# Optimization experiments

Measured on AMD Instinct MI355X. Metric: run time of the kernel, lower is better.

Reference implementation:

```python
import jax, jax.numpy as jnp
import numpy as np
import math

B, T = 16, 512
P = 256          # num_memory_positions
E = 128          # embedding_dim
NB = 4           # num_beings
K = 4            # attention_radius
TEMP = 8.0       # attention_temperature
PHI = 1.618033988749895


def setup_inputs() -> dict:
    key = jax.random.key(0)
    ks = jax.random.split(key, 8)
    x = jax.random.normal(ks[0], (B, T, 8), jnp.float32)
    W_in = jax.random.normal(ks[1], (8, E), jnp.float32) * 0.1
    b_in = jnp.zeros((E,), jnp.float32)
    W_out = jax.random.normal(ks[2], (E, 8), jnp.float32) * 0.1
    b_out = jnp.zeros((8,), jnp.float32)
    W_p = jax.random.normal(ks[3], (E, E), jnp.float32) * (1.0 / np.sqrt(E))
    b_p = jnp.zeros((E,), jnp.float32)
    ptr_dest = jax.random.uniform(ks[4], (NB, P), jnp.float32) * P
    jump_W = jax.random.normal(ks[5], (NB, E), jnp.float32) * 0.1
    jump_b = jnp.zeros((NB,), jnp.float32)
    ctx_strength = jnp.full((NB,), 0.2, jnp.float32)
    pe = np.zeros((NB, E), np.float32)
    for i in range(NB):
        ph = i * PHI
        v = []
        for h in range(1, 9):
            v += [math.sin(h * ph), math.cos(h * ph)]
        pe[i, :16] = v  # phase_embedding padded with zeros to E (E >= 16)
    phase_bias = jnp.asarray(pe)
    seg = P / NB
    pointer_init = jax.random.uniform(ks[6], (NB, B), jnp.float32) * seg + jnp.arange(NB, dtype=jnp.float32)[:, None] * seg
    return dict(x=x, W_in=W_in, b_in=b_in, W_out=W_out, b_out=b_out,
                W_p=W_p, b_p=b_p, ptr_dest=ptr_dest, jump_W=jump_W,
                jump_b=jump_b, ctx_strength=ctx_strength,
                phase_bias=phase_bias, pointer_init=pointer_init)


def _forward(x, W_in, b_in, W_out, b_out, W_p, b_p, ptr_dest, jump_W,
             jump_b, ctx_strength, phase_bias, pointer_init):
    offsets = jnp.arange(-K, K + 1)          # [W]
    b_ix = jnp.arange(B)                     # [B]
    half = P / 2.0
    ring0 = jnp.zeros((B, P, E), x.dtype)
    hid0 = jnp.zeros((NB, B, E), x.dtype)

    def step(carry, x_t):
        ring, ptrs, hids = carry
        inp = x_t @ W_in + b_in              # [B,E]
        outs, new_ptrs, new_hids = [], [], []
        for i in range(NB):                  # beings sequential (share ring)
            ptr, hid = ptrs[i], hids[i]
            base = jnp.clip(jnp.floor(ptr).astype(jnp.int32), 0, P - 1)
            idx = (base[:, None] + offsets[None, :]) % P            # [B,W]
            delta = jnp.mod(idx.astype(x_t.dtype) - ptr[:, None] + half, P) - half
            w = jax.nn.softmax(-(delta ** 2) / TEMP, axis=1)         # [B,W]
            nbhd = ring[b_ix[:, None], idx]                          # [B,W,E]
            ctx = jnp.sum(w[..., None] * nbhd, axis=1)               # [B,E]
            comb = inp + jax.nn.sigmoid(ctx_strength[i]) * ctx + 0.1 * phase_bias[i]
            s = jnp.tanh(comb + hid)
            s = jnp.tanh(s @ W_p + b_p)      # depth-1 = 1 processing layer
            ring = ring.at[b_ix[:, None], idx].add(w[..., None] * s[:, None, :])
            cur = jnp.clip(ptr.astype(jnp.int32), 0, P - 1)
            jump_target = ptr_dest[i][cur]                           # [B]
            probs = jax.nn.sigmoid(s @ jump_W[i] + jump_b[i])        # [B]
            hard = (probs > 0.5).astype(s.dtype)
            should_jump = hard - jax.lax.stop_gradient(probs) + probs
            walk = (ptr + 1.0) % P
            new_ptrs.append(jnp.where(should_jump > 0.5, jump_target, walk))
            new_hids.append(s)
            outs.append(s @ W_out + b_out)                           # [B,8]
        out_t = jnp.mean(jnp.stack(outs), axis=0)                    # [B,8] (training-mode mean)
        return (ring, jnp.stack(new_ptrs), jnp.stack(new_hids)), out_t

    _, ys = jax.lax.scan(step, (ring0, pointer_init, hid0), jnp.swapaxes(x, 0, 1))
    return jnp.swapaxes(ys, 0, 1)            # [B,T,8]


def reference(x, W_in, b_in, W_out, b_out, W_p, b_p, ptr_dest, jump_W,
              jump_b, ctx_strength, phase_bias, pointer_init):
    return _forward(x, W_in, b_in, W_out, b_out, W_p, b_p, ptr_dest,
                    jump_W, jump_b, ctx_strength, phase_bias, pointer_init)
```

## Files before the change

kernel.cpp:

```cpp
#include <hip/hip_runtime.h>
#include <cmath>

namespace {
constexpr int B_ = 16, T_ = 512, P_ = 256, E_ = 128, NB_ = 4, K_ = 4;

__device__ __forceinline__ float rcpf(float x) { return __builtin_amdgcn_rcpf(x); }
__device__ __forceinline__ float fast_tanh(float x) {
    float a = fabsf(x);
    float t = __expf(-2.0f * a);
    float r = 1.0f - 2.0f * t * rcpf(1.0f + t);
    return copysignf(r, x);
}
__device__ __forceinline__ float redkq(float v) {
    v += __shfl_xor(v, 16);
    v += __shfl_xor(v, 32);
    return v;
}
__device__ __forceinline__ float sel4(int kq, float a, float b, float c, float d) {
    const float t0 = (kq & 1) ? b : a;
    const float t1 = (kq & 1) ? d : c;
    return (kq & 2) ? t1 : t0;
}
}

__global__ __launch_bounds__(256, 1)
void swarm_ring_kernel(const float* __restrict__ x,
                       const float* __restrict__ W_in,
                       const float* __restrict__ b_in,
                       const float* __restrict__ W_out,
                       const float* __restrict__ b_out,
                       const float* __restrict__ W_p,
                       const float* __restrict__ b_p,
                       const float* __restrict__ ptr_dest,
                       const float* __restrict__ jump_W,
                       const float* __restrict__ jump_b,
                       const float* __restrict__ ctx_strength,
                       const float* __restrict__ phase_bias,
                       const float* __restrict__ pointer_init,
                       float* __restrict__ out)
{
    __shared__ alignas(16) float ring[P_ * E_];
    __shared__ alignas(16) float s1p[NB_ * E_];
    __shared__ alignas(16) float red[16];
    __shared__ alignas(16) float hist[16][132];
    __shared__ alignas(16) float wout_s[8][132];

    const int tid = threadIdx.x;
    const int b   = blockIdx.x;
    const int w   = tid >> 6;
    const int l   = tid & 63;
    const int sub = l & 15;
    const int kq  = l >> 4;
    const int e0  = ((w << 4) | sub) << 1;

    for (int k4 = tid; k4 < P_ * E_ / 4; k4 += 256)
        ((float4*)ring)[k4] = make_float4(0.f, 0.f, 0.f, 0.f);
    for (int idx = tid; idx < 8 * E_; idx += 256) {
        const int m = idx >> 7, ee = idx & 127;
        wout_s[m][ee] = W_out[ee * 8 + m] * 0.25f;
    }

    float2 wp2[32];
    #pragma unroll
    for (int kk = 0; kk < 32; ++kk)
        wp2[kk] = *(const float2*)(W_p + (kq * 32 + kk) * E_ + e0);

    const float2 bin2 = *(const float2*)(b_in + e0);
    const float2 bp2  = *(const float2*)(b_p + e0);
    const float  bout_m = b_out[tid & 7];

    float2 pb2[NB_], jw2[NB_], hid2[NB_];
    float  sigc[NB_], jb_r[NB_], ptrv[NB_];
    #pragma unroll
    for (int i = 0; i < NB_; ++i) {
        const float2 pb = *(const float2*)(phase_bias + i * E_ + e0);
        pb2[i] = make_float2(0.1f * pb.x, 0.1f * pb.y);
        jw2[i] = *(const float2*)(jump_W + i * E_ + e0);
        sigc[i] = 1.0f / (1.0f + __expf(-ctx_strength[i]));
        jb_r[i] = jump_b[i];
        hid2[i] = make_float2(0.f, 0.f);
        ptrv[i] = pointer_init[i * B_ + b];
    }

    const float* xb = x + (size_t)b * T_ * 8;
    float xt[8];
    {
        float4 a0 = ((const float4*)xb)[0], a1 = ((const float4*)xb)[1];
        xt[0]=a0.x; xt[1]=a0.y; xt[2]=a0.z; xt[3]=a0.w;
        xt[4]=a1.x; xt[5]=a1.y; xt[6]=a1.z; xt[7]=a1.w;
    }

    const float Cw1 = 0.8824969f, Cw2 = 0.60653066f, Cw3 = 0.32465247f, Cw4 = 0.13533528f;
    const float Dw1 = 0.7788008f, Dw2 = 0.36787944f, Dw3 = 0.105399225f, Dw4 = 0.018315639f;

    __syncthreads();

    for (int t = 0; t < T_; ++t) {
        int   baseA[NB_];
        float fA[NB_], psinv[NB_], jt[NB_], wgt[NB_][9];
        #pragma unroll
        for (int i = 0; i < NB_; ++i) {
            const float p = ptrv[i];
            const int base = (int)p;
            baseA[i] = base;
            jt[i] = ptr_dest[i * P_ + base];
            const float f = p - (float)base;
            fA[i] = f;
            const float r  = __expf(0.25f * f);
            const float r2 = r * r, r3 = r2 * r, r4 = r2 * r2;
            const float ri = rcpf(r), ri2 = ri * ri, ri3 = ri2 * ri, ri4 = ri2 * ri2;
            const float p0 = Cw4*ri4, p1 = Cw3*ri3, p2 = Cw2*ri2, p3 = Cw1*ri, p4 = 1.0f,
                        p5 = Cw1*r,  p6 = Cw2*r2,  p7 = Cw3*r3,  p8 = Cw4*r4;
            const float sum = ((p0+p1)+(p2+p3)) + ((p4+p5)+(p6+p7)) + p8;
            const float inv = rcpf(sum);
            psinv[i] = inv;
            wgt[i][0]=p0*inv; wgt[i][1]=p1*inv; wgt[i][2]=p2*inv; wgt[i][3]=p3*inv;
            wgt[i][4]=p4*inv; wgt[i][5]=p5*inv; wgt[i][6]=p6*inv; wgt[i][7]=p7*inv;
            wgt[i][8]=p8*inv;
        }

        int ddm[NB_][NB_];
        int lev[NB_];
        lev[0] = 0;
        #pragma unroll
        for (int j = 1; j < NB_; ++j) {
            int mx = -1;
            #pragma unroll
            for (int i = 0; i < j; ++i) {
                const int dd = ((baseA[j] - baseA[i] + 128) & 255) - 128;
                ddm[j][i] = dd;
                if (dd >= -8 && dd <= 8 && lev[i] > mx) mx = lev[i];
            }
            lev[j] = mx + 1;
        }
        const int nlev = 1 + ((lev[1] > lev[0] ? lev[1] : lev[0]) > (lev[2] > lev[3] ? lev[2] : lev[3])
                              ? (lev[1] > lev[0] ? lev[1] : lev[0])
                              : (lev[2] > lev[3] ? lev[2] : lev[3]));

        float  ws0[NB_], ws1[NB_];
        float2 ctxp2[NB_];
        #pragma unroll
        for (int i = 0; i < NB_; ++i) {
            ws0[i] = sel4(kq, wgt[i][0], wgt[i][1], wgt[i][2], wgt[i][3]);
            ws1[i] = sel4(kq, wgt[i][4], wgt[i][5], wgt[i][6], wgt[i][7]);
            const int r0 = (baseA[i] + kq - K_) & (P_ - 1);
            const int r1 = (baseA[i] + kq + 4 - K_) & (P_ - 1);
            const float2 g0 = *(const float2*)(ring + r0 * E_ + e0);
            const float2 g1 = *(const float2*)(ring + r1 * E_ + e0);
            float cx = fmaf(ws1[i], g1.x, ws0[i] * g0.x);
            float cy = fmaf(ws1[i], g1.y, ws0[i] * g0.y);
            if (kq == 0) {
                const int r2 = (baseA[i] + 8 - K_) & (P_ - 1);
                const float2 g2 = *(const float2*)(ring + r2 * E_ + e0);
                cx = fmaf(wgt[i][8], g2.x, cx);
                cy = fmaf(wgt[i][8], g2.y, cy);
            }
            ctxp2[i] = make_float2(redkq(cx), redkq(cy));
        }

        float coefm[NB_][NB_];
        #pragma unroll
        for (int j = 1; j < NB_; ++j) {
            #pragma unroll
            for (int i = 0; i < j; ++i) {
                const int dd = ddm[j][i];
                float c = 0.f;
                if (dd >= -8 && dd <= 8) {
                    const float A = (float)dd - fA[i];
                    const float s  = __expf(-0.25f * (A - fA[j]));
                    const float G  = __expf(0.125f * (fA[i] * fA[i] - A * A));
                    const float s2p = s * s, s3p = s2p * s, s4p = s2p * s2p;
                    const float si = rcpf(s), si2 = si * si, si3 = si2 * si, si4 = si2 * si2;
                    float acc = 0.f;
                    acc += (dd >= 0)              ? Dw4 * si4 : 0.f;
                    acc += (dd >= -1 && dd <= 7)  ? Dw3 * si3 : 0.f;
                    acc += (dd >= -2 && dd <= 6)  ? Dw2 * si2 : 0.f;
                    acc += (dd >= -3 && dd <= 5)  ? Dw1 * si  : 0.f;
                    acc += (dd >= -4 && dd <= 4)  ? 1.0f      : 0.f;
                    acc += (dd >= -5 && dd <= 3)  ? Dw1 * s   : 0.f;
                    acc += (dd >= -6 && dd <= 2)  ? Dw2 * s2p : 0.f;
                    acc += (dd >= -7 && dd <= 1)  ? Dw3 * s3p : 0.f;
                    acc += (dd <= 0)              ? Dw4 * s4p : 0.f;
                    c = psinv[i] * psinv[j] * G * acc;
                }
                coefm[j][i] = c;
            }
        }

        float2 inp2 = bin2;
        #pragma unroll
        for (int k = 0; k < 8; ++k) {
            const float2 wk = *(const float2*)(W_in + k * E_ + e0);
            inp2.x = fmaf(xt[k], wk.x, inp2.x);
            inp2.y = fmaf(xt[k], wk.y, inp2.y);
        }

        float xtn[8];
        if (t + 1 < T_) {
            float4 a0 = ((const float4*)(xb + (t + 1) * 8))[0];
            float4 a1 = ((const float4*)(xb + (t + 1) * 8))[1];
            xtn[0]=a0.x; xtn[1]=a0.y; xtn[2]=a0.z; xtn[3]=a0.w;
            xtn[4]=a1.x; xtn[5]=a1.y; xtn[6]=a1.z; xtn[7]=a1.w;
        } else {
            #pragma unroll
            for (int k = 0; k < 8; ++k) xtn[k] = 0.f;
        }

        float2 sv2[NB_];
        #pragma unroll
        for (int j = 0; j < NB_; ++j) sv2[j] = make_float2(0.f, 0.f);

        for (int L = 0; L < nlev; ++L) {
            #pragma unroll
            for (int j = 0; j < NB_; ++j) {
                if (lev[j] != L) continue;
                float2 ctx = ctxp2[j];
                #pragma unroll
                for (int i = 0; i < j; ++i) {
                    ctx.x = fmaf(coefm[j][i], sv2[i].x, ctx.x);
                    ctx.y = fmaf(coefm[j][i], sv2[i].y, ctx.y);
                }
                float2 s1;
                s1.x = fast_tanh(fmaf(sigc[j], ctx.x, inp2.x + pb2[j].x + hid2[j].x));
                s1.y = fast_tanh(fmaf(sigc[j], ctx.y, inp2.y + pb2[j].y + hid2[j].y));
                if (kq == 0) *(float2*)(s1p + j * E_ + e0) = s1;
            }
            __syncthreads();

            #pragma unroll
            for (int j = 0; j < NB_; ++j) {
                if (lev[j] != L) continue;
                const float4* sp = (const float4*)(s1p + j * E_) + kq * 8;
                float ax = 0.f, ay = 0.f;
                #pragma unroll
                for (int kk = 0; kk < 8; ++kk) {
                    const float4 sq = sp[kk];
                    const float2 wa = wp2[4 * kk + 0], wb = wp2[4 * kk + 1];
                    const float2 wc = wp2[4 * kk + 2], wd = wp2[4 * kk + 3];
                    ax = fmaf(sq.x, wa.x, ax); ay = fmaf(sq.x, wa.y, ay);
                    ax = fmaf(sq.y, wb.x, ax); ay = fmaf(sq.y, wb.y, ay);
                    ax = fmaf(sq.z, wc.x, ax); ay = fmaf(sq.z, wc.y, ay);
                    ax = fmaf(sq.w, wd.x, ax); ay = fmaf(sq.w, wd.y, ay);
                }
                float2 s2;
                s2.x = fast_tanh(redkq(ax) + bp2.x);
                s2.y = fast_tanh(redkq(ay) + bp2.y);
                sv2[j] = s2; hid2[j] = s2;

                const int r0 = (baseA[j] + kq - K_) & (P_ - 1);
                float2* q0 = (float2*)(ring + r0 * E_ + e0);
                float2 v0 = *q0;
                v0.x = fmaf(ws0[j], s2.x, v0.x); v0.y = fmaf(ws0[j], s2.y, v0.y);
                *q0 = v0;
                const int r1 = (baseA[j] + kq + 4 - K_) & (P_ - 1);
                float2* q1 = (float2*)(ring + r1 * E_ + e0);
                float2 v1 = *q1;
                v1.x = fmaf(ws1[j], s2.x, v1.x); v1.y = fmaf(ws1[j], s2.y, v1.y);
                *q1 = v1;
                if (kq == 0) {
                    const int r2 = (baseA[j] + 8 - K_) & (P_ - 1);
                    float2* q2 = (float2*)(ring + r2 * E_ + e0);
                    float2 v2 = *q2;
                    v2.x = fmaf(wgt[j][8], s2.x, v2.x); v2.y = fmaf(wgt[j][8], s2.y, v2.y);
                    *q2 = v2;
                }
            }
        }

        {
            float vj0 = fmaf(sv2[0].y, jw2[0].y, sv2[0].x * jw2[0].x);
            float vj1 = fmaf(sv2[1].y, jw2[1].y, sv2[1].x * jw2[1].x);
            float vj2 = fmaf(sv2[2].y, jw2[2].y, sv2[2].x * jw2[2].x);
            float vj3 = fmaf(sv2[3].y, jw2[3].y, sv2[3].x * jw2[3].x);
            #pragma unroll
            for (int off = 1; off < 16; off <<= 1) {
                vj0 += __shfl_xor(vj0, off);
                vj1 += __shfl_xor(vj1, off);
                vj2 += __shfl_xor(vj2, off);
                vj3 += __shfl_xor(vj3, off);
            }
            if (l == 0)
                ((float4*)red)[w] = make_float4(vj0, vj1, vj2, vj3);
        }

        {
            float2 ssum2;
            ssum2.x = (sv2[0].x + sv2[1].x) + (sv2[2].x + sv2[3].x);
            ssum2.y = (sv2[0].y + sv2[1].y) + (sv2[2].y + sv2[3].y);
            if (kq == 0) *(float2*)(&hist[t & 15][e0]) = ssum2;
        }

        __syncthreads();

        {
            const float4 r0 = ((const float4*)red)[0];
            const float4 r1 = ((const float4*)red)[1];
            const float4 r2 = ((const float4*)red)[2];
            const float4 r3 = ((const float4*)red)[3];
            const float zz[4] = {
                ((r0.x + r1.x) + (r2.x + r3.x)) + jb_r[0],
                ((r0.y + r1.y) + (r2.y + r3.y)) + jb_r[1],
                ((r0.z + r1.z) + (r2.z + r3.z)) + jb_r[2],
                ((r0.w + r1.w) + (r2.w + r3.w)) + jb_r[3]};
            #pragma unroll
            for (int i = 0; i < NB_; ++i) {
                float np;
                if (zz[i] > 0.0f) np = jt[i];
                else { np = ptrv[i] + 1.0f; if (np >= 256.0f) np -= 256.0f; }
                ptrv[i] = np;
            }
        }

        if ((t & 7) == 7 && tid < 64) {
            const int tt = tid >> 3;
            const int m  = tid & 7;
            const float* hrow = hist[(t - 7 + tt) & 15];
            const float* wrow = wout_s[m];
            float acc = 0.f;
            #pragma unroll
            for (int q = 0; q < 32; ++q) {
                const float4 h4 = ((const float4*)hrow)[q];
                const float4 w4 = ((const float4*)wrow)[q];
                acc += ((h4.x * w4.x + h4.y * w4.y) + (h4.z * w4.z + h4.w * w4.w));
            }
            out[((size_t)b * T_ + (t - 7 + tt)) * 8 + m] = acc + bout_m;
        }

        #pragma unroll
        for (int k = 0; k < 8; ++k) xt[k] = xtn[k];
    }
}

extern "C" void kernel_launch(void* const* d_in, const int* in_sizes, int n_in,
                              void* d_out, int out_size, void* d_ws, size_t ws_size,
                              hipStream_t stream) {
    (void)in_sizes; (void)n_in; (void)out_size; (void)d_ws; (void)ws_size;
    swarm_ring_kernel<<<dim3(B_), dim3(256), 0, stream>>>(
        (const float*)d_in[0],  (const float*)d_in[1],  (const float*)d_in[2],
        (const float*)d_in[3],  (const float*)d_in[4],  (const float*)d_in[5],
        (const float*)d_in[6],  (const float*)d_in[7],  (const float*)d_in[8],
        (const float*)d_in[9],  (const float*)d_in[10], (const float*)d_in[11],
        (const float*)d_in[12], (float*)d_out);
}
```

Baseline: 2.060 ms.

## Split beings across two 256-thread groups in a 512-thread block

The block grows from 256 to 512 threads and each half owns two of the four beings, so per-being context gathers, tanh and W_p matvec work are split between the two halves. Cross-group dependencies go through a shared svp buffer, and hist becomes per-group with the halves summed at output time. This aims to halve per-thread serial work per timestep. In exchange it adds an extra barrier between dependency levels and more shared-memory traffic, and with only 16 blocks the gain depends on whether the extra waves hide latency.

```diff
diff --git a/kernel.cpp b/kernel.cpp
--- a/kernel.cpp
+++ b/kernel.cpp
@@ -23,7 +23,7 @@
 }
 }
 
-__global__ __launch_bounds__(256, 1)
+__global__ __launch_bounds__(512, 1)
 void swarm_ring_kernel(const float* __restrict__ x,
                        const float* __restrict__ W_in,
                        const float* __restrict__ b_in,
@@ -41,21 +41,24 @@
 {
     __shared__ alignas(16) float ring[P_ * E_];
     __shared__ alignas(16) float s1p[NB_ * E_];
+    __shared__ alignas(16) float svp[NB_ * E_];
     __shared__ alignas(16) float red[16];
-    __shared__ alignas(16) float hist[16][132];
+    __shared__ alignas(16) float hist2[2][16][132];
     __shared__ alignas(16) float wout_s[8][132];
 
     const int tid = threadIdx.x;
     const int b   = blockIdx.x;
     const int w   = tid >> 6;
     const int l   = tid & 63;
+    const int grp = w >> 2;
+    const int wl  = w & 3;
     const int sub = l & 15;
     const int kq  = l >> 4;
-    const int e0  = ((w << 4) | sub) << 1;
-
-    for (int k4 = tid; k4 < P_ * E_ / 4; k4 += 256)
+    const int e0  = ((wl << 4) | sub) << 1;
+
+    for (int k4 = tid; k4 < P_ * E_ / 4; k4 += 512)
         ((float4*)ring)[k4] = make_float4(0.f, 0.f, 0.f, 0.f);
-    for (int idx = tid; idx < 8 * E_; idx += 256) {
+    for (int idx = tid; idx < 8 * E_; idx += 512) {
         const int m = idx >> 7, ee = idx & 127;
         wout_s[m][ee] = W_out[ee * 8 + m] * 0.25f;
     }
@@ -69,17 +72,22 @@
     const float2 bp2  = *(const float2*)(b_p + e0);
     const float  bout_m = b_out[tid & 7];
 
-    float2 pb2[NB_], jw2[NB_], hid2[NB_];
-    float  sigc[NB_], jb_r[NB_], ptrv[NB_];
+    float jb_r[NB_], ptrv[NB_];
     #pragma unroll
     for (int i = 0; i < NB_; ++i) {
-        const float2 pb = *(const float2*)(phase_bias + i * E_ + e0);
-        pb2[i] = make_float2(0.1f * pb.x, 0.1f * pb.y);
-        jw2[i] = *(const float2*)(jump_W + i * E_ + e0);
-        sigc[i] = 1.0f / (1.0f + __expf(-ctx_strength[i]));
         jb_r[i] = jump_b[i];
-        hid2[i] = make_float2(0.f, 0.f);
         ptrv[i] = pointer_init[i * B_ + b];
+    }
+    float2 pb2L[2], jw2L[2], hid2L[2];
+    float  sigcL[2];
+    #pragma unroll
+    for (int lb = 0; lb < 2; ++lb) {
+        const int j = (grp << 1) + lb;
+        const float2 pb = *(const float2*)(phase_bias + j * E_ + e0);
+        pb2L[lb] = make_float2(0.1f * pb.x, 0.1f * pb.y);
+        jw2L[lb] = *(const float2*)(jump_W + j * E_ + e0);
+        sigcL[lb] = 1.0f / (1.0f + __expf(-ctx_strength[j]));
+        hid2L[lb] = make_float2(0.f, 0.f);
     }
 
     const float* xb = x + (size_t)b * T_ * 8;
@@ -96,15 +104,20 @@
     __syncthreads();
 
     for (int t = 0; t < T_; ++t) {
-        int   baseA[NB_];
-        float fA[NB_], psinv[NB_], jt[NB_], wgt[NB_][9];
+        int   base[NB_];
+        float fA[NB_], psinv[NB_], jt4[NB_];
+        float wgtL[2][9];
+        #pragma unroll
+        for (int lb = 0; lb < 2; ++lb)
+            #pragma unroll
+            for (int o = 0; o < 9; ++o) wgtL[lb][o] = 0.f;
         #pragma unroll
         for (int i = 0; i < NB_; ++i) {
             const float p = ptrv[i];
-            const int base = (int)p;
-            baseA[i] = base;
-            jt[i] = ptr_dest[i * P_ + base];
-            const float f = p - (float)base;
+            const int bs = (int)p;
+            base[i] = bs;
+            jt4[i] = ptr_dest[i * P_ + bs];
+            const float f = p - (float)bs;
             fA[i] = f;
             const float r  = __expf(0.25f * f);
             const float r2 = r * r, r3 = r2 * r, r4 = r2 * r2;
@@ -114,12 +127,14 @@
             const float sum = ((p0+p1)+(p2+p3)) + ((p4+p5)+(p6+p7)) + p8;
             const float inv = rcpf(sum);
             psinv[i] = inv;
-            wgt[i][0]=p0*inv; wgt[i][1]=p1*inv; wgt[i][2]=p2*inv; wgt[i][3]=p3*inv;
-            wgt[i][4]=p4*inv; wgt[i][5]=p5*inv; wgt[i][6]=p6*inv; wgt[i][7]=p7*inv;
-            wgt[i][8]=p8*inv;
-        }
-
-        int ddm[NB_][NB_];
+            if ((i >> 1) == grp) {
+                const int lb = i & 1;
+                wgtL[lb][0]=p0*inv; wgtL[lb][1]=p1*inv; wgtL[lb][2]=p2*inv;
+                wgtL[lb][3]=p3*inv; wgtL[lb][4]=p4*inv; wgtL[lb][5]=p5*inv;
+                wgtL[lb][6]=p6*inv; wgtL[lb][7]=p7*inv; wgtL[lb][8]=p8*inv;
+            }
+        }
+
         int lev[NB_];
         lev[0] = 0;
         #pragma unroll
@@ -127,64 +142,71 @@
             int mx = -1;
             #pragma unroll
             for (int i = 0; i < j; ++i) {
-                const int dd = ((baseA[j] - baseA[i] + 128) & 255) - 128;
-                ddm[j][i] = dd;
+                const int dd = ((base[j] - base[i] + 128) & 255) - 128;
                 if (dd >= -8 && dd <= 8 && lev[i] > mx) mx = lev[i];
             }
             lev[j] = mx + 1;
         }
-        const int nlev = 1 + ((lev[1] > lev[0] ? lev[1] : lev[0]) > (lev[2] > lev[3] ? lev[2] : lev[3])
-                              ? (lev[1] > lev[0] ? lev[1] : lev[0])
-                              : (lev[2] > lev[3] ? lev[2] : lev[3]));
-
-        float  ws0[NB_], ws1[NB_];
-        float2 ctxp2[NB_];
-        #pragma unroll
-        for (int i = 0; i < NB_; ++i) {
-            ws0[i] = sel4(kq, wgt[i][0], wgt[i][1], wgt[i][2], wgt[i][3]);
-            ws1[i] = sel4(kq, wgt[i][4], wgt[i][5], wgt[i][6], wgt[i][7]);
-            const int r0 = (baseA[i] + kq - K_) & (P_ - 1);
-            const int r1 = (baseA[i] + kq + 4 - K_) & (P_ - 1);
+        const int m01 = lev[1] > lev[0] ? lev[1] : lev[0];
+        const int m23 = lev[2] > lev[3] ? lev[2] : lev[3];
+        const int nlev = 1 + (m01 > m23 ? m01 : m23);
+        const int levL[2] = {grp ? lev[2] : lev[0], grp ? lev[3] : lev[1]};
+        const int baseL[2] = {grp ? base[2] : base[0], grp ? base[3] : base[1]};
+        const float fL[2] = {grp ? fA[2] : fA[0], grp ? fA[3] : fA[1]};
+        const float psL[2] = {grp ? psinv[2] : psinv[0], grp ? psinv[3] : psinv[1]};
+
+        float cm[2][3];
+        bool  needcL[2] = {false, false};
+        #pragma unroll
+        for (int lb = 0; lb < 2; ++lb) {
+            #pragma unroll
+            for (int i = 0; i < 3; ++i) {
+                cm[lb][i] = 0.f;
+                const bool valid = grp ? (i < 2 + lb) : (lb == 1 && i == 0);
+                if (valid) {
+                    const int dd = ((baseL[lb] - base[i] + 128) & 255) - 128;
+                    if (dd >= -8 && dd <= 8) {
+                        const float A = (float)dd - fA[i];
+                        const float s  = __expf(-0.25f * (A - fL[lb]));
+                        const float G  = __expf(0.125f * (fA[i] * fA[i] - A * A));
+                        const float s2p = s * s, s3p = s2p * s, s4p = s2p * s2p;
+                        const float si = rcpf(s), si2 = si * si, si3 = si2 * si, si4 = si2 * si2;
+                        float acc = 0.f;
+                        acc += (dd >= 0)              ? Dw4 * si4 : 0.f;
+                        acc += (dd >= -1 && dd <= 7)  ? Dw3 * si3 : 0.f;
+                        acc += (dd >= -2 && dd <= 6)  ? Dw2 * si2 : 0.f;
+                        acc += (dd >= -3 && dd <= 5)  ? Dw1 * si  : 0.f;
+                        acc += (dd >= -4 && dd <= 4)  ? 1.0f      : 0.f;
+                        acc += (dd >= -5 && dd <= 3)  ? Dw1 * s   : 0.f;
+                        acc += (dd >= -6 && dd <= 2)  ? Dw2 * s2p : 0.f;
+                        acc += (dd >= -7 && dd <= 1)  ? Dw3 * s3p : 0.f;
+                        acc += (dd <= 0)              ? Dw4 * s4p : 0.f;
+                        cm[lb][i] = psinv[i] * psL[lb] * G * acc;
+                        needcL[lb] = true;
+                    }
+                }
+            }
+        }
+
+        float  ws0L[2], ws1L[2];
+        float2 ctxpL[2];
+        #pragma unroll
+        for (int lb = 0; lb < 2; ++lb) {
+            ws0L[lb] = sel4(kq, wgtL[lb][0], wgtL[lb][1], wgtL[lb][2], wgtL[lb][3]);
+            ws1L[lb] = sel4(kq, wgtL[lb][4], wgtL[lb][5], wgtL[lb][6], wgtL[lb][7]);
+            const int r0 = (baseL[lb] + kq - K_) & (P_ - 1);
+            const int r1 = (baseL[lb] + kq + 4 - K_) & (P_ - 1);
             const float2 g0 = *(const float2*)(ring + r0 * E_ + e0);
             const float2 g1 = *(const float2*)(ring + r1 * E_ + e0);
-            float cx = fmaf(ws1[i], g1.x, ws0[i] * g0.x);
-            float cy = fmaf(ws1[i], g1.y, ws0[i] * g0.y);
+            float cx = fmaf(ws1L[lb], g1.x, ws0L[lb] * g0.x);
+            float cy = fmaf(ws1L[lb], g1.y, ws0L[lb] * g0.y);
             if (kq == 0) {
-                const int r2 = (baseA[i] + 8 - K_) & (P_ - 1);
+                const int r2 = (baseL[lb] + 8 - K_) & (P_ - 1);
                 const float2 g2 = *(const float2*)(ring + r2 * E_ + e0);
-                cx = fmaf(wgt[i][8], g2.x, cx);
-                cy = fmaf(wgt[i][8], g2.y, cy);
-            }
-            ctxp2[i] = make_float2(redkq(cx), redkq(cy));
-        }
-
-        float coefm[NB_][NB_];
-        #pragma unroll
-        for (int j = 1; j < NB_; ++j) {
-            #pragma unroll
-            for (int i = 0; i < j; ++i) {
-                const int dd = ddm[j][i];
-                float c = 0.f;
-                if (dd >= -8 && dd <= 8) {
-                    const float A = (float)dd - fA[i];
-                    const float s  = __expf(-0.25f * (A - fA[j]));
-                    const float G  = __expf(0.125f * (fA[i] * fA[i] - A * A));
-                    const float s2p = s * s, s3p = s2p * s, s4p = s2p * s2p;
-                    const float si = rcpf(s), si2 = si * si, si3 = si2 * si, si4 = si2 * si2;
-                    float acc = 0.f;
-                    acc += (dd >= 0)              ? Dw4 * si4 : 0.f;
-                    acc += (dd >= -1 && dd <= 7)  ? Dw3 * si3 : 0.f;
-                    acc += (dd >= -2 && dd <= 6)  ? Dw2 * si2 : 0.f;
-                    acc += (dd >= -3 && dd <= 5)  ? Dw1 * si  : 0.f;
-                    acc += (dd >= -4 && dd <= 4)  ? 1.0f      : 0.f;
-                    acc += (dd >= -5 && dd <= 3)  ? Dw1 * s   : 0.f;
-                    acc += (dd >= -6 && dd <= 2)  ? Dw2 * s2p : 0.f;
-                    acc += (dd >= -7 && dd <= 1)  ? Dw3 * s3p : 0.f;
-                    acc += (dd <= 0)              ? Dw4 * s4p : 0.f;
-                    c = psinv[i] * psinv[j] * G * acc;
-                }
-                coefm[j][i] = c;
-            }
+                cx = fmaf(wgtL[lb][8], g2.x, cx);
+                cy = fmaf(wgtL[lb][8], g2.y, cy);
+            }
+            ctxpL[lb] = make_float2(redkq(cx), redkq(cy));
         }
 
         float2 inp2 = bin2;
@@ -206,31 +228,40 @@
             for (int k = 0; k < 8; ++k) xtn[k] = 0.f;
         }
 
-        float2 sv2[NB_];
-        #pragma unroll
-        for (int j = 0; j < NB_; ++j) sv2[j] = make_float2(0.f, 0.f);
+        float2 sv2L[2] = {make_float2(0.f, 0.f), make_float2(0.f, 0.f)};
 
         for (int L = 0; L < nlev; ++L) {
             #pragma unroll
-            for (int j = 0; j < NB_; ++j) {
-                if (lev[j] != L) continue;
-                float2 ctx = ctxp2[j];
-                #pragma unroll
-                for (int i = 0; i < j; ++i) {
-                    ctx.x = fmaf(coefm[j][i], sv2[i].x, ctx.x);
-                    ctx.y = fmaf(coefm[j][i], sv2[i].y, ctx.y);
+            for (int lb = 0; lb < 2; ++lb) {
+                if (levL[lb] != L) continue;
+                const int jg = (grp << 1) + lb;
+                float2 ctx = ctxpL[lb];
+                if (needcL[lb]) {
+                    #pragma unroll
+                    for (int i = 0; i < 3; ++i) {
+                        const bool valid = grp ? (i < 2 + lb) : (lb == 1 && i == 0);
+                        if (valid) {
+                            const bool sameGrp = (i >> 1) == grp;
+                            float2 si;
+                            if (sameGrp) si = sv2L[0];
+                            else         si = *(const float2*)(svp + i * E_ + e0);
+                            ctx.x = fmaf(cm[lb][i], si.x, ctx.x);
+                            ctx.y = fmaf(cm[lb][i], si.y, ctx.y);
+                        }
+                    }
                 }
                 float2 s1;
-                s1.x = fast_tanh(fmaf(sigc[j], ctx.x, inp2.x + pb2[j].x + hid2[j].x));
-                s1.y = fast_tanh(fmaf(sigc[j], ctx.y, inp2.y + pb2[j].y + hid2[j].y));
-                if (kq == 0) *(float2*)(s1p + j * E_ + e0) = s1;
+                s1.x = fast_tanh(fmaf(sigcL[lb], ctx.x, inp2.x + pb2L[lb].x + hid2L[lb].x));
+                s1.y = fast_tanh(fmaf(sigcL[lb], ctx.y, inp2.y + pb2L[lb].y + hid2L[lb].y));
+                if (kq == 0) *(float2*)(s1p + jg * E_ + e0) = s1;
             }
             __syncthreads();
 
             #pragma unroll
-            for (int j = 0; j < NB_; ++j) {
-                if (lev[j] != L) continue;
-                const float4* sp = (const float4*)(s1p + j * E_) + kq * 8;
+            for (int lb = 0; lb < 2; ++lb) {
+                if (levL[lb] != L) continue;
+                const int jg = (grp << 1) + lb;
+                const float4* sp = (const float4*)(s1p + jg * E_) + kq * 8;
                 float ax = 0.f, ay = 0.f;
                 #pragma unroll
                 for (int kk = 0; kk < 8; ++kk) {
@@ -245,67 +276,62 @@
                 float2 s2;
                 s2.x = fast_tanh(redkq(ax) + bp2.x);
                 s2.y = fast_tanh(redkq(ay) + bp2.y);
-                sv2[j] = s2; hid2[j] = s2;
-
-                const int r0 = (baseA[j] + kq - K_) & (P_ - 1);
+                sv2L[lb] = s2; hid2L[lb] = s2;
+                if (kq == 0) *(float2*)(svp + jg * E_ + e0) = s2;
+
+                const int r0 = (baseL[lb] + kq - K_) & (P_ - 1);
                 float2* q0 = (float2*)(ring + r0 * E_ + e0);
                 float2 v0 = *q0;
-                v0.x = fmaf(ws0[j], s2.x, v0.x); v0.y = fmaf(ws0[j], s2.y, v0.y);
+                v0.x = fmaf(ws0L[lb], s2.x, v0.x); v0.y = fmaf(ws0L[lb], s2.y, v0.y);
                 *q0 = v0;
-                const int r1 = (baseA[j] + kq + 4 - K_) & (P_ - 1);
+                const int r1 = (baseL[lb] + kq + 4 - K_) & (P_ - 1);
                 float2* q1 = (float2*)(ring + r1 * E_ + e0);
                 float2 v1 = *q1;
-                v1.x = fmaf(ws1[j], s2.x, v1.x); v1.y = fmaf(ws1[j], s2.y, v1.y);
+                v1.x = fmaf(ws1L[lb], s2.x, v1.x); v1.y = fmaf(ws1L[lb], s2.y, v1.y);
                 *q1 = v1;
                 if (kq == 0) {
-                    const int r2 = (baseA[j] + 8 - K_) & (P_ - 1);
+                    const int r2 = (baseL[lb] + 8 - K_) & (P_ - 1);
                     float2* q2 = (float2*)(ring + r2 * E_ + e0);
                     float2 v2 = *q2;
-                    v2.x = fmaf(wgt[j][8], s2.x, v2.x); v2.y = fmaf(wgt[j][8], s2.y, v2.y);
+                    v2.x = fmaf(wgtL[lb][8], s2.x, v2.x); v2.y = fmaf(wgtL[lb][8], s2.y, v2.y);
                     *q2 = v2;
                 }
             }
+            if (L + 1 < nlev) __syncthreads();
         }
 
         {
-            float vj0 = fmaf(sv2[0].y, jw2[0].y, sv2[0].x * jw2[0].x);
-            float vj1 = fmaf(sv2[1].y, jw2[1].y, sv2[1].x * jw2[1].x);
-            float vj2 = fmaf(sv2[2].y, jw2[2].y, sv2[2].x * jw2[2].x);
-            float vj3 = fmaf(sv2[3].y, jw2[3].y, sv2[3].x * jw2[3].x);
+            float vjA = fmaf(sv2L[0].y, jw2L[0].y, sv2L[0].x * jw2L[0].x);
+            float vjB = fmaf(sv2L[1].y, jw2L[1].y, sv2L[1].x * jw2L[1].x);
             #pragma unroll
             for (int off = 1; off < 16; off <<= 1) {
-                vj0 += __shfl_xor(vj0, off);
-                vj1 += __shfl_xor(vj1, off);
-                vj2 += __shfl_xor(vj2, off);
-                vj3 += __shfl_xor(vj3, off);
-            }
-            if (l == 0)
-                ((float4*)red)[w] = make_float4(vj0, vj1, vj2, vj3);
+                vjA += __shfl_xor(vjA, off);
+                vjB += __shfl_xor(vjB, off);
+            }
+            if (l == 0) ((float2*)red)[w] = make_float2(vjA, vjB);
         }
 
         {
-            float2 ssum2;
-            ssum2.x = (sv2[0].x + sv2[1].x) + (sv2[2].x + sv2[3].x);
-            ssum2.y = (sv2[0].y + sv2[1].y) + (sv2[2].y + sv2[3].y);
-            if (kq == 0) *(float2*)(&hist[t & 15][e0]) = ssum2;
+            float2 ss2;
+            ss2.x = sv2L[0].x + sv2L[1].x;
+            ss2.y = sv2L[0].y + sv2L[1].y;
+            if (kq == 0) *(float2*)(&hist2[grp][t & 15][e0]) = ss2;
         }
 
         __syncthreads();
 
         {
-            const float4 r0 = ((const float4*)red)[0];
-            const float4 r1 = ((const float4*)red)[1];
-            const float4 r2 = ((const float4*)red)[2];
-            const float4 r3 = ((const float4*)red)[3];
-            const float zz[4] = {
-                ((r0.x + r1.x) + (r2.x + r3.x)) + jb_r[0],
-                ((r0.y + r1.y) + (r2.y + r3.y)) + jb_r[1],
-                ((r0.z + r1.z) + (r2.z + r3.z)) + jb_r[2],
-                ((r0.w + r1.w) + (r2.w + r3.w)) + jb_r[3]};
+            float zz[NB_];
+            #pragma unroll
+            for (int i = 0; i < NB_; ++i) {
+                const int g = i >> 1, o = i & 1;
+                zz[i] = ((red[2 * (4 * g + 0) + o] + red[2 * (4 * g + 1) + o]) +
+                         (red[2 * (4 * g + 2) + o] + red[2 * (4 * g + 3) + o])) + jb_r[i];
+            }
             #pragma unroll
             for (int i = 0; i < NB_; ++i) {
                 float np;
-                if (zz[i] > 0.0f) np = jt[i];
+                if (zz[i] > 0.0f) np = jt4[i];
                 else { np = ptrv[i] + 1.0f; if (np >= 256.0f) np -= 256.0f; }
                 ptrv[i] = np;
             }
@@ -314,14 +340,18 @@
         if ((t & 7) == 7 && tid < 64) {
             const int tt = tid >> 3;
             const int m  = tid & 7;
-            const float* hrow = hist[(t - 7 + tt) & 15];
+            const int row = (t - 7 + tt) & 15;
+            const float* hA = hist2[0][row];
+            const float* hB = hist2[1][row];
             const float* wrow = wout_s[m];
             float acc = 0.f;
             #pragma unroll
             for (int q = 0; q < 32; ++q) {
-                const float4 h4 = ((const float4*)hrow)[q];
+                const float4 a4 = ((const float4*)hA)[q];
+                const float4 b4 = ((const float4*)hB)[q];
                 const float4 w4 = ((const float4*)wrow)[q];
-                acc += ((h4.x * w4.x + h4.y * w4.y) + (h4.z * w4.z + h4.w * w4.w));
+                acc += (((a4.x + b4.x) * w4.x + (a4.y + b4.y) * w4.y) +
+                        ((a4.z + b4.z) * w4.z + (a4.w + b4.w) * w4.w));
             }
             out[((size_t)b * T_ + (t - 7 + tt)) * 8 + m] = acc + bout_m;
         }
@@ -335,7 +365,7 @@
                               void* d_out, int out_size, void* d_ws, size_t ws_size,
                               hipStream_t stream) {
     (void)in_sizes; (void)n_in; (void)out_size; (void)d_ws; (void)ws_size;
-    swarm_ring_kernel<<<dim3(B_), dim3(256), 0, stream>>>(
+    swarm_ring_kernel<<<dim3(B_), dim3(512), 0, stream>>>(
         (const float*)d_in[0],  (const float*)d_in[1],  (const float*)d_in[2],
         (const float*)d_in[3],  (const float*)d_in[4],  (const float*)d_in[5],
         (const float*)d_in[6],  (const float*)d_in[7],  (const float*)d_in[8],
```

After: 2.085 ms. No clear change (+1.2%).

## Speculatively precompute both next-pointer candidates' weights before the jump decision

Applied to the files above, without the earlier changes.

Per-being pointer state (base, fraction, normalized attention weights, jump target lookup) is now computed for both possible next pointers (walk and jump) during the current step, before the block-wide jump decision is known. After the barrier, the correct candidate is chosen with selects. This takes the exp/rcp chain and the dependent ptr_dest global load off the critical path at the start of each step. The projection dot product is also split into two accumulator chains to shorten the FMA dependency. The cost is doubled weight computation and much higher register pressure, which may cause spills.

```diff
diff --git a/kernel.cpp b/kernel.cpp
--- a/kernel.cpp
+++ b/kernel.cpp
@@ -70,7 +70,7 @@
     const float  bout_m = b_out[tid & 7];
 
     float2 pb2[NB_], jw2[NB_], hid2[NB_];
-    float  sigc[NB_], jb_r[NB_], ptrv[NB_];
+    float  sigc[NB_], jb_r[NB_];
     #pragma unroll
     for (int i = 0; i < NB_; ++i) {
         const float2 pb = *(const float2*)(phase_bias + i * E_ + e0);
@@ -79,7 +79,33 @@
         sigc[i] = 1.0f / (1.0f + __expf(-ctx_strength[i]));
         jb_r[i] = jump_b[i];
         hid2[i] = make_float2(0.f, 0.f);
-        ptrv[i] = pointer_init[i * B_ + b];
+    }
+
+    const float Cw1 = 0.8824969f, Cw2 = 0.60653066f, Cw3 = 0.32465247f, Cw4 = 0.13533528f;
+    const float Dw1 = 0.7788008f, Dw2 = 0.36787944f, Dw3 = 0.105399225f, Dw4 = 0.018315639f;
+
+    float ptrv[NB_], fA[NB_], psinv[NB_], jt4[NB_], wgt[NB_][9];
+    int   base[NB_];
+    #pragma unroll
+    for (int i = 0; i < NB_; ++i) {
+        const float p = pointer_init[i * B_ + b];
+        ptrv[i] = p;
+        const int bs = (int)p;
+        base[i] = bs;
+        jt4[i] = ptr_dest[i * P_ + bs];
+        const float f = p - (float)bs;
+        fA[i] = f;
+        const float r  = __expf(0.25f * f);
+        const float r2 = r * r, r3 = r2 * r, r4 = r2 * r2;
+        const float ri = rcpf(r), ri2 = ri * ri, ri3 = ri2 * ri, ri4 = ri2 * ri2;
+        const float p0 = Cw4*ri4, p1 = Cw3*ri3, p2 = Cw2*ri2, p3 = Cw1*ri, p4 = 1.0f,
+                    p5 = Cw1*r,  p6 = Cw2*r2,  p7 = Cw3*r3,  p8 = Cw4*r4;
+        const float sum = ((p0+p1)+(p2+p3)) + ((p4+p5)+(p6+p7)) + p8;
+        const float inv = rcpf(sum);
+        psinv[i] = inv;
+        wgt[i][0]=p0*inv; wgt[i][1]=p1*inv; wgt[i][2]=p2*inv; wgt[i][3]=p3*inv;
+        wgt[i][4]=p4*inv; wgt[i][5]=p5*inv; wgt[i][6]=p6*inv; wgt[i][7]=p7*inv;
+        wgt[i][8]=p8*inv;
     }
 
     const float* xb = x + (size_t)b * T_ * 8;
@@ -90,36 +116,9 @@
         xt[4]=a1.x; xt[5]=a1.y; xt[6]=a1.z; xt[7]=a1.w;
     }
 
-    const float Cw1 = 0.8824969f, Cw2 = 0.60653066f, Cw3 = 0.32465247f, Cw4 = 0.13533528f;
-    const float Dw1 = 0.7788008f, Dw2 = 0.36787944f, Dw3 = 0.105399225f, Dw4 = 0.018315639f;
-
     __syncthreads();
 
     for (int t = 0; t < T_; ++t) {
-        int   baseA[NB_];
-        float fA[NB_], psinv[NB_], jt[NB_], wgt[NB_][9];
-        #pragma unroll
-        for (int i = 0; i < NB_; ++i) {
-            const float p = ptrv[i];
-            const int base = (int)p;
-            baseA[i] = base;
-            jt[i] = ptr_dest[i * P_ + base];
-            const float f = p - (float)base;
-            fA[i] = f;
-            const float r  = __expf(0.25f * f);
-            const float r2 = r * r, r3 = r2 * r, r4 = r2 * r2;
-            const float ri = rcpf(r), ri2 = ri * ri, ri3 = ri2 * ri, ri4 = ri2 * ri2;
-            const float p0 = Cw4*ri4, p1 = Cw3*ri3, p2 = Cw2*ri2, p3 = Cw1*ri, p4 = 1.0f,
-                        p5 = Cw1*r,  p6 = Cw2*r2,  p7 = Cw3*r3,  p8 = Cw4*r4;
-            const float sum = ((p0+p1)+(p2+p3)) + ((p4+p5)+(p6+p7)) + p8;
-            const float inv = rcpf(sum);
-            psinv[i] = inv;
-            wgt[i][0]=p0*inv; wgt[i][1]=p1*inv; wgt[i][2]=p2*inv; wgt[i][3]=p3*inv;
-            wgt[i][4]=p4*inv; wgt[i][5]=p5*inv; wgt[i][6]=p6*inv; wgt[i][7]=p7*inv;
-            wgt[i][8]=p8*inv;
-        }
-
-        int ddm[NB_][NB_];
         int lev[NB_];
         lev[0] = 0;
         #pragma unroll
@@ -127,15 +126,14 @@
             int mx = -1;
             #pragma unroll
             for (int i = 0; i < j; ++i) {
-                const int dd = ((baseA[j] - baseA[i] + 128) & 255) - 128;
-                ddm[j][i] = dd;
+                const int dd = ((base[j] - base[i] + 128) & 255) - 128;
                 if (dd >= -8 && dd <= 8 && lev[i] > mx) mx = lev[i];
             }
             lev[j] = mx + 1;
         }
-        const int nlev = 1 + ((lev[1] > lev[0] ? lev[1] : lev[0]) > (lev[2] > lev[3] ? lev[2] : lev[3])
-                              ? (lev[1] > lev[0] ? lev[1] : lev[0])
-                              : (lev[2] > lev[3] ? lev[2] : lev[3]));
+        const int m01 = lev[1] > lev[0] ? lev[1] : lev[0];
+        const int m23 = lev[2] > lev[3] ? lev[2] : lev[3];
+        const int nlev = 1 + (m01 > m23 ? m01 : m23);
 
         float  ws0[NB_], ws1[NB_];
         float2 ctxp2[NB_];
@@ -143,14 +141,14 @@
         for (int i = 0; i < NB_; ++i) {
             ws0[i] = sel4(kq, wgt[i][0], wgt[i][1], wgt[i][2], wgt[i][3]);
             ws1[i] = sel4(kq, wgt[i][4], wgt[i][5], wgt[i][6], wgt[i][7]);
-            const int r0 = (baseA[i] + kq - K_) & (P_ - 1);
-            const int r1 = (baseA[i] + kq + 4 - K_) & (P_ - 1);
+            const int r0 = (base[i] + kq - K_) & (P_ - 1);
+            const int r1 = (base[i] + kq + 4 - K_) & (P_ - 1);
             const float2 g0 = *(const float2*)(ring + r0 * E_ + e0);
             const float2 g1 = *(const float2*)(ring + r1 * E_ + e0);
             float cx = fmaf(ws1[i], g1.x, ws0[i] * g0.x);
             float cy = fmaf(ws1[i], g1.y, ws0[i] * g0.y);
             if (kq == 0) {
-                const int r2 = (baseA[i] + 8 - K_) & (P_ - 1);
+                const int r2 = (base[i] + 8 - K_) & (P_ - 1);
                 const float2 g2 = *(const float2*)(ring + r2 * E_ + e0);
                 cx = fmaf(wgt[i][8], g2.x, cx);
                 cy = fmaf(wgt[i][8], g2.y, cy);
@@ -163,7 +161,7 @@
         for (int j = 1; j < NB_; ++j) {
             #pragma unroll
             for (int i = 0; i < j; ++i) {
-                const int dd = ddm[j][i];
+                const int dd = ((base[j] - base[i] + 128) & 255) - 128;
                 float c = 0.f;
                 if (dd >= -8 && dd <= 8) {
                     const float A = (float)dd - fA[i];
@@ -206,6 +204,35 @@
             for (int k = 0; k < 8; ++k) xtn[k] = 0.f;
         }
 
+        float pC[2][NB_], fC[2][NB_], psC[2][NB_], jtC[2][NB_], wgtC[2][NB_][9];
+        int   baseC[2][NB_];
+        #pragma unroll
+        for (int c = 0; c < 2; ++c) {
+            #pragma unroll
+            for (int i = 0; i < NB_; ++i) {
+                float p;
+                if (c == 0) { p = ptrv[i] + 1.0f; if (p >= 256.0f) p -= 256.0f; }
+                else        { p = jt4[i]; }
+                pC[c][i] = p;
+                const int bs = (int)p;
+                baseC[c][i] = bs;
+                jtC[c][i] = ptr_dest[i * P_ + bs];
+                const float f = p - (float)bs;
+                fC[c][i] = f;
+                const float r  = __expf(0.25f * f);
+                const float r2 = r * r, r3 = r2 * r, r4 = r2 * r2;
+                const float ri = rcpf(r), ri2 = ri * ri, ri3 = ri2 * ri, ri4 = ri2 * ri2;
+                const float p0 = Cw4*ri4, p1 = Cw3*ri3, p2 = Cw2*ri2, p3 = Cw1*ri, p4 = 1.0f,
+                            p5 = Cw1*r,  p6 = Cw2*r2,  p7 = Cw3*r3,  p8 = Cw4*r4;
+                const float sum = ((p0+p1)+(p2+p3)) + ((p4+p5)+(p6+p7)) + p8;
+                const float inv = rcpf(sum);
+                psC[c][i] = inv;
+                wgtC[c][i][0]=p0*inv; wgtC[c][i][1]=p1*inv; wgtC[c][i][2]=p2*inv;
+                wgtC[c][i][3]=p3*inv; wgtC[c][i][4]=p4*inv; wgtC[c][i][5]=p5*inv;
+                wgtC[c][i][6]=p6*inv; wgtC[c][i][7]=p7*inv; wgtC[c][i][8]=p8*inv;
+            }
+        }
+
         float2 sv2[NB_];
         #pragma unroll
         for (int j = 0; j < NB_; ++j) sv2[j] = make_float2(0.f, 0.f);
@@ -231,34 +258,44 @@
             for (int j = 0; j < NB_; ++j) {
                 if (lev[j] != L) continue;
                 const float4* sp = (const float4*)(s1p + j * E_) + kq * 8;
-                float ax = 0.f, ay = 0.f;
+                float ax0 = 0.f, ay0 = 0.f, ax1 = 0.f, ay1 = 0.f;
                 #pragma unroll
-                for (int kk = 0; kk < 8; ++kk) {
+                for (int kk = 0; kk < 4; ++kk) {
                     const float4 sq = sp[kk];
                     const float2 wa = wp2[4 * kk + 0], wb = wp2[4 * kk + 1];
                     const float2 wc = wp2[4 * kk + 2], wd = wp2[4 * kk + 3];
-                    ax = fmaf(sq.x, wa.x, ax); ay = fmaf(sq.x, wa.y, ay);
-                    ax = fmaf(sq.y, wb.x, ax); ay = fmaf(sq.y, wb.y, ay);
-                    ax = fmaf(sq.z, wc.x, ax); ay = fmaf(sq.z, wc.y, ay);
-                    ax = fmaf(sq.w, wd.x, ax); ay = fmaf(sq.w, wd.y, ay);
+                    ax0 = fmaf(sq.x, wa.x, ax0); ay0 = fmaf(sq.x, wa.y, ay0);
+                    ax0 = fmaf(sq.y, wb.x, ax0); ay0 = fmaf(sq.y, wb.y, ay0);
+                    ax0 = fmaf(sq.z, wc.x, ax0); ay0 = fmaf(sq.z, wc.y, ay0);
+                    ax0 = fmaf(sq.w, wd.x, ax0); ay0 = fmaf(sq.w, wd.y, ay0);
+                }
+                #pragma unroll
+                for (int kk = 4; kk < 8; ++kk) {
+                    const float4 sq = sp[kk];
+                    const float2 wa = wp2[4 * kk + 0], wb = wp2[4 * kk + 1];
+                    const float2 wc = wp2[4 * kk + 2], wd = wp2[4 * kk + 3];
+                    ax1 = fmaf(sq.x, wa.x, ax1); ay1 = fmaf(sq.x, wa.y, ay1);
+                    ax1 = fmaf(sq.y, wb.x, ax1); ay1 = fmaf(sq.y, wb.y, ay1);
+                    ax1 = fmaf(sq.z, wc.x, ax1); ay1 = fmaf(sq.z, wc.y, ay1);
+                    ax1 = fmaf(sq.w, wd.x, ax1); ay1 = fmaf(sq.w, wd.y, ay1);
                 }
                 float2 s2;
-                s2.x = fast_tanh(redkq(ax) + bp2.x);
-                s2.y = fast_tanh(redkq(ay) + bp2.y);
+                s2.x = fast_tanh(redkq(ax0 + ax1) + bp2.x);
+                s2.y = fast_tanh(redkq(ay0 + ay1) + bp2.y);
                 sv2[j] = s2; hid2[j] = s2;
 
-                const int r0 = (baseA[j] + kq - K_) & (P_ - 1);
+                const int r0 = (base[j] + kq - K_) & (P_ - 1);
                 float2* q0 = (float2*)(ring + r0 * E_ + e0);
                 float2 v0 = *q0;
                 v0.x = fmaf(ws0[j], s2.x, v0.x); v0.y = fmaf(ws0[j], s2.y, v0.y);
                 *q0 = v0;
-                const int r1 = (baseA[j] + kq + 4 - K_) & (P_ - 1);
+                const int r1 = (base[j] + kq + 4 - K_) & (P_ - 1);
                 float2* q1 = (float2*)(ring + r1 * E_ + e0);
                 float2 v1 = *q1;
                 v1.x = fmaf(ws1[j], s2.x, v1.x); v1.y = fmaf(ws1[j], s2.y, v1.y);
                 *q1 = v1;
                 if (kq == 0) {
-                    const int r2 = (baseA[j] + 8 - K_) & (P_ - 1);
+                    const int r2 = (base[j] + 8 - K_) & (P_ - 1);
                     float2* q2 = (float2*)(ring + r2 * E_ + e0);
                     float2 v2 = *q2;
                     v2.x = fmaf(wgt[j][8], s2.x, v2.x); v2.y = fmaf(wgt[j][8], s2.y, v2.y);
@@ -297,17 +334,23 @@
             const float4 r1 = ((const float4*)red)[1];
             const float4 r2 = ((const float4*)red)[2];
             const float4 r3 = ((const float4*)red)[3];
-            const float zz[4] = {
-                ((r0.x + r1.x) + (r2.x + r3.x)) + jb_r[0],
-                ((r0.y + r1.y) + (r2.y + r3.y)) + jb_r[1],
-                ((r0.z + r1.z) + (r2.z + r3.z)) + jb_r[2],
-                ((r0.w + r1.w) + (r2.w + r3.w)) + jb_r[3]};
+            const float zz0 = ((r0.x + r1.x) + (r2.x + r3.x)) + jb_r[0];
+            const float zz1 = ((r0.y + r1.y) + (r2.y + r3.y)) + jb_r[1];
+            const float zz2 = ((r0.z + r1.z) + (r2.z + r3.z)) + jb_r[2];
+            const float zz3 = ((r0.w + r1.w) + (r2.w + r3.w)) + jb_r[3];
+            const bool jm[4] = {zz0 > 0.f, zz1 > 0.f, zz2 > 0.f, zz3 > 0.f};
             #pragma unroll
             for (int i = 0; i < NB_; ++i) {
-                float np;
-                if (zz[i] > 0.0f) np = jt[i];
-                else { np = ptrv[i] + 1.0f; if (np >= 256.0f) np -= 256.0f; }
-                ptrv[i] = np;
+                const int c = jm[i] ? 1 : 0;
+                base[i]  = jm[i] ? baseC[1][i] : baseC[0][i];
+                ptrv[i]  = jm[i] ? pC[1][i]   : pC[0][i];
+                fA[i]    = jm[i] ? fC[1][i]   : fC[0][i];
+                psinv[i] = jm[i] ? psC[1][i]  : psC[0][i];
+                jt4[i]   = jm[i] ? jtC[1][i]  : jtC[0][i];
+                #pragma unroll
+                for (int o = 0; o < 9; ++o)
+                    wgt[i][o] = jm[i] ? wgtC[1][i][o] : wgtC[0][i][o];
+                (void)c;
             }
         }
 
```

New measurement: 2.262 ms. 1.1x slower.
